# Performance work log

Hardware: AMD Instinct MI355X
Metric: run time of the kernel (lower is better)

The kernel has to match this reference:

```python
import jax, jax.numpy as jnp
import numpy as np

N = 16384        # num_variables
C = 512          # number of budget constraints
K = 64           # variables per constraint (uniform constraint_sizes)
STRIDE = 32      # overlapping windows -> every variable has degree 2
BATCH = 64
BUDGET = 8.0     # budgets[i]
MAX_ITER = 25    # ADMM / AD3 iterations
RHO = 1.0        # penalty parameter
BISECT = 25      # bisection steps for the budget projection threshold


def setup_inputs() -> dict:
    key = jax.random.key(0)
    scores = jax.random.normal(key, (BATCH, N), dtype=jnp.float32)
    # constraint_sets: constraint c covers variables [c*STRIDE, c*STRIDE+K) mod N
    base = (np.arange(C)[:, None] * STRIDE + np.arange(K)[None, :]) % N
    constraint_idx = jnp.asarray(base, dtype=jnp.int32)  # [C, K]
    return {"scores": scores, "constraint_idx": constraint_idx}


def _proj_budget(a, budget):
    """Project rows a[..., K] onto {z in [0,1]^K : sum(z) <= budget}."""
    z0 = jnp.clip(a, 0.0, 1.0)
    feasible = jnp.sum(z0, -1, keepdims=True) <= budget
    # bisection for tau with sum(clip(a - tau, 0, 1)) == budget
    a_sg = jax.lax.stop_gradient(a)
    lo = jnp.min(a_sg, -1, keepdims=True) - 1.0
    hi = jnp.max(a_sg, -1, keepdims=True)
    for _ in range(BISECT):  # fixed small algorithmic loop
        mid = 0.5 * (lo + hi)
        s = jnp.sum(jnp.clip(a_sg - mid, 0.0, 1.0), -1, keepdims=True)
        lo = jnp.where(s > budget, mid, lo)
        hi = jnp.where(s > budget, hi, mid)
    tau0 = 0.5 * (lo + hi)
    # one implicit (Newton) correction so tau is differentiable in a
    active = ((a_sg - tau0 > 0.0) & (a_sg - tau0 < 1.0)).astype(a.dtype)
    n_act = jnp.maximum(jnp.sum(active, -1, keepdims=True), 1.0)
    g = jnp.sum(jnp.clip(a - tau0, 0.0, 1.0), -1, keepdims=True) - budget
    tau = tau0 + g / n_act
    z_proj = jnp.clip(a - tau, 0.0, 1.0)
    return jnp.where(feasible, z0, z_proj)


def _forward(scores, constraint_idx):
    B, n_vars = scores.shape
    idx = constraint_idx  # [C, K]
    deg = jnp.zeros((n_vars,), scores.dtype).at[idx.reshape(-1)].add(1.0)
    deg_safe = jnp.maximum(deg, 1.0)

    def u_update(z, lam):
        # u = (theta + A^T(rho*z - lam)) / (rho * deg), boxed to [0,1]
        msg = RHO * z - lam                                   # [B,C,K]
        t = jnp.zeros_like(scores).at[:, idx].add(msg)        # A^T scatter
        u = (scores + t) / (RHO * deg_safe)
        u = jnp.clip(u, 0.0, 1.0)
        # unconstrained variables: LP optimum is the indicator of theta > 0
        return jnp.where(deg > 0.0, u, (scores > 0.0).astype(scores.dtype))

    def step(carry, _):
        z, lam = carry
        u = u_update(z, lam)
        Au = u[:, idx]                                        # gather [B,C,K]
        z_new = _proj_budget(Au + lam / RHO, BUDGET)
        lam_new = lam + RHO * (Au - z_new)
        return (z_new, lam_new), None

    z0 = jnp.zeros((B, idx.shape[0], idx.shape[1]), scores.dtype)
    lam0 = jnp.zeros_like(z0)
    (z, lam), _ = jax.lax.scan(step, (z0, lam0), None, length=MAX_ITER)
    return u_update(z, lam)


def reference(scores, constraint_idx):
    return _forward(scores, constraint_idx)
```

## Files before the change

kernel.cpp:

```cpp
#include <hip/hip_runtime.h>
#include <math.h>


#define NGLOB   16384
#define KD      64
#define MAXIT   25
#define NBIS    11
#define BUDGETF 8.0f
#define CHUNK   128
#define HALO    25
#define NCREAL  (CHUNK + 2*HALO)
#define NROWP   192
#define NTHREADS 768
#define MSGROWS (NROWP + 2)
#define RS4     17
#define OFF4    (MSGROWS * RS4)

typedef float v4f __attribute__((ext_vector_type(4)));
typedef float v2f __attribute__((ext_vector_type(2)));

__device__ __forceinline__ float clip01(float x) {
    return __builtin_amdgcn_fmed3f(x, 0.0f, 1.0f);
}
__device__ __forceinline__ v4f clipv(v4f x) {
    v4f r;
    r.x = clip01(x.x); r.y = clip01(x.y); r.z = clip01(x.z); r.w = clip01(x.w);
    return r;
}
__device__ __forceinline__ v4f minv(v4f a, v4f b) {
    v4f r; r.x=fminf(a.x,b.x); r.y=fminf(a.y,b.y); r.z=fminf(a.z,b.z); r.w=fminf(a.w,b.w); return r;
}
__device__ __forceinline__ v4f maxv(v4f a, v4f b) {
    v4f r; r.x=fmaxf(a.x,b.x); r.y=fmaxf(a.y,b.y); r.z=fmaxf(a.z,b.z); r.w=fmaxf(a.w,b.w); return r;
}
__device__ __forceinline__ float sum16(v4f a, v4f b, v4f c, v4f d) {
    v4f t = (a + b) + (c + d);
    v2f u = t.xy + t.zw;
    return u.x + u.y;
}
__device__ __forceinline__ float min16(v4f a, v4f b, v4f c, v4f d) {
    v4f t = minv(minv(a, b), minv(c, d));
    return fminf(fminf(t.x, t.y), fminf(t.z, t.w));
}
__device__ __forceinline__ float max16(v4f a, v4f b, v4f c, v4f d) {
    v4f t = maxv(maxv(a, b), maxv(c, d));
    return fmaxf(fmaxf(t.x, t.y), fmaxf(t.z, t.w));
}
__device__ __forceinline__ float ind01(float x) { return (x > 0.0f && x < 1.0f) ? 1.0f : 0.0f; }

template<int CTRL>
__device__ __forceinline__ float dpp_mv(float x) {
    union U { float f; int i; } s, r;
    s.f = x;
    r.i = __builtin_amdgcn_update_dpp(0, s.i, CTRL, 0xf, 0xf, true);
    return r.f;
}
__device__ __forceinline__ float g4_sum(float x) {
    x += dpp_mv<0xB1>(x);
    x += dpp_mv<0x4E>(x);
    return x;
}
__device__ __forceinline__ float g4_min(float x) {
    x = fminf(x, dpp_mv<0xB1>(x));
    x = fminf(x, dpp_mv<0x4E>(x));
    return x;
}
__device__ __forceinline__ float g4_max(float x) {
    x = fmaxf(x, dpp_mv<0xB1>(x));
    x = fmaxf(x, dpp_mv<0x4E>(x));
    return x;
}

__global__ void __launch_bounds__(NTHREADS, 3)
lpsmap_kernel(const float* __restrict__ scores, float* __restrict__ out) {
    __shared__ float msg[2 * OFF4 * 4];
    v4f* msg4 = (v4f*)msg;

    const int tid  = threadIdx.x;
    const int wid  = tid >> 6;
    const int lane = tid & 63;
    const int g    = lane >> 2;
    const int l4   = lane & 3;
    const int khi  = l4 >> 1;
    const int lc   = l4 & 1;
    const int b    = blockIdx.x >> 2;
    const int c0v  = (blockIdx.x & 3) * (CHUNK * 32);
    const float* sb = scores + b * NGLOB;

    for (int i = tid; i < 2 * OFF4; i += NTHREADS)
        msg4[i] = v4f{0.0f, 0.0f, 0.0f, 0.0f};

    const int rr = wid * 16 + g;
    const int i1 = (rr + khi + 1) * RS4 + 4 * lc;
    const int i2 = (rr + khi) * RS4 + 8 + 4 * lc;
    const int iw = (rr + 1) * RS4 + 4 * l4;

    v4f sch[4], lam[4], av[4];
    {
        const int off = (c0v - HALO * 32 + rr * 32 + 16 * l4 + NGLOB) & (NGLOB - 1);
        const v4f* gp = (const v4f*)(sb + off);
        #pragma unroll
        for (int q = 0; q < 4; ++q) {
            sch[q] = gp[q] * 0.5f;
            lam[q] = v4f{0.0f, 0.0f, 0.0f, 0.0f};
        }
    }

    __syncthreads();

    int roff = 0;
    #pragma unroll 1
    for (int it = 0; it < MAXIT; ++it) {
        const v4f* mr = msg4 + roff;
        v4f*       mw = msg4 + (roff ^ OFF4);

        #pragma unroll
        for (int q = 0; q < 4; ++q) {
            v4f m1 = mr[i1 + q];
            v4f m2 = mr[i2 + q];
            v4f u  = clipv((m1 + m2) * 0.5f + sch[q]);
            av[q]  = u + lam[q];
        }

        float lo = g4_min(min16(av[0], av[1], av[2], av[3])) - 1.0f;
        float hi = g4_max(max16(av[0], av[1], av[2], av[3]));

        #pragma unroll 1
        for (int j = 0; j < NBIS; ++j) {
            float mid = 0.5f * (lo + hi);
            float s = g4_sum(sum16(clipv(av[0] - mid), clipv(av[1] - mid),
                                   clipv(av[2] - mid), clipv(av[3] - mid)));
            bool gt = s > BUDGETF;
            lo = gt ? mid : lo;
            hi = gt ? hi : mid;
        }

        {
            float tau0 = 0.5f * (lo + hi);
            v4f d0 = av[0] - tau0, d1 = av[1] - tau0;
            v4f d2 = av[2] - tau0, d3 = av[3] - tau0;
            float gs = g4_sum(sum16(clipv(d0), clipv(d1), clipv(d2), clipv(d3))) - BUDGETF;
            float act = (((ind01(d0.x) + ind01(d0.y)) + (ind01(d0.z) + ind01(d0.w)))
                       + ((ind01(d1.x) + ind01(d1.y)) + (ind01(d1.z) + ind01(d1.w))))
                      + (((ind01(d2.x) + ind01(d2.y)) + (ind01(d2.z) + ind01(d2.w)))
                       + ((ind01(d3.x) + ind01(d3.y)) + (ind01(d3.z) + ind01(d3.w))));
            float nact = fmaxf(g4_sum(act), 1.0f);
            float tau = tau0 + gs * __builtin_amdgcn_rcpf(nact);
            tau = fmaxf(tau, 0.0f);
            #pragma unroll
            for (int q = 0; q < 4; ++q) {
                v4f z  = clipv(av[q] - tau);
                lam[q] = av[q] - z;
                mw[iw + q] = 2.0f * z - av[q];
            }
        }
        roff ^= OFF4;
        __syncthreads();
    }

    if (tid < CHUNK * 32 / 8) {
        const v4f* mr = msg4 + roff;
        const int j   = tid * 8;
        const int vl  = HALO * 32 + j;
        const int rrl = vl >> 5;
        const int cq  = (vl & 31) >> 2;
        v4f m1a = mr[(rrl + 1) * RS4 + cq],   m1b = mr[(rrl + 1) * RS4 + cq + 1];
        v4f m2a = mr[rrl * RS4 + 8 + cq],     m2b = mr[rrl * RS4 + 8 + cq + 1];
        const v4f* gp = (const v4f*)(sb + c0v + j);
        v4f u0 = clipv((gp[0] + m1a + m2a) * 0.5f);
        v4f u1 = clipv((gp[1] + m1b + m2b) * 0.5f);
        v4f* op = (v4f*)(out + (size_t)b * NGLOB + c0v + j);
        op[0] = u0;
        op[1] = u1;
    }
}

extern "C" void kernel_launch(void* const* d_in, const int* in_sizes, int n_in,
                              void* d_out, int out_size, void* d_ws, size_t ws_size,
                              hipStream_t stream) {
    const float* scores = (const float*)d_in[0];
    float* out = (float*)d_out;
    dim3 grid(64 * 4);
    dim3 block(NTHREADS);
    lpsmap_kernel<<<grid, block, 0, stream>>>(scores, out);
}
```

Before: 135.2 us.

## Exchange ADMM messages between lanes with ds_bpermute, shared memory only at wave edges

Each thread now keeps its own outgoing message in registers. It gets the overlapping neighbour's message through ds_bpermute lane shuffles instead of writing and reading a full double-buffered shared-memory message array. Only the edge lanes of each wave publish to and read from a small shared buffer, which cuts LDS traffic and footprint per iteration. The final output pass is also changed to use the same register-plus-shuffle path. bpermute still goes through the LDS crossbar, and the edge lanes are indexed in an intricate way.

Result: slower. 139.0 us (+2.8%).

```diff
diff --git a/kernel.cpp b/kernel.cpp
--- a/kernel.cpp
+++ b/kernel.cpp
@@ -3,18 +3,15 @@
 
 
 #define NGLOB   16384
-#define KD      64
 #define MAXIT   25
 #define NBIS    11
 #define BUDGETF 8.0f
 #define CHUNK   128
 #define HALO    25
-#define NCREAL  (CHUNK + 2*HALO)
-#define NROWP   192
 #define NTHREADS 768
-#define MSGROWS (NROWP + 2)
-#define RS4     17
-#define OFF4    (MSGROWS * RS4)
+#define NW      12
+#define PSLOTS  (NW + 2)
+#define PUBV    (PSLOTS * 2 * 2 * 4)
 
 typedef float v4f __attribute__((ext_vector_type(4)));
 typedef float v2f __attribute__((ext_vector_type(2)));
@@ -70,56 +67,68 @@
     x = fmaxf(x, dpp_mv<0x4E>(x));
     return x;
 }
+__device__ __forceinline__ v4f bperm4(int addr, v4f x) {
+    union { v4f v; int i[4]; } a, r;
+    a.v = x;
+    #pragma unroll
+    for (int t = 0; t < 4; ++t)
+        r.i[t] = __builtin_amdgcn_ds_bpermute(addr, a.i[t]);
+    return r.v;
+}
 
 __global__ void __launch_bounds__(NTHREADS, 3)
 lpsmap_kernel(const float* __restrict__ scores, float* __restrict__ out) {
-    __shared__ float msg[2 * OFF4 * 4];
-    v4f* msg4 = (v4f*)msg;
+    __shared__ v4f pub[2 * PUBV];
 
     const int tid  = threadIdx.x;
     const int wid  = tid >> 6;
     const int lane = tid & 63;
     const int g    = lane >> 2;
     const int l4   = lane & 3;
-    const int khi  = l4 >> 1;
-    const int lc   = l4 & 1;
     const int b    = blockIdx.x >> 2;
     const int c0v  = (blockIdx.x & 3) * (CHUNK * 32);
     const float* sb = scores + b * NGLOB;
 
-    for (int i = tid; i < 2 * OFF4; i += NTHREADS)
-        msg4[i] = v4f{0.0f, 0.0f, 0.0f, 0.0f};
+    if (tid < 2 * PUBV) pub[tid] = v4f{0.0f, 0.0f, 0.0f, 0.0f};
 
     const int rr = wid * 16 + g;
-    const int i1 = (rr + khi + 1) * RS4 + 4 * lc;
-    const int i2 = (rr + khi) * RS4 + 8 + 4 * lc;
-    const int iw = (rr + 1) * RS4 + 4 * l4;
+    const int bp_addr = ((((l4 < 2) ? (lane - 2) : (lane + 2)) & 63) << 2);
+    const bool edge = (lane < 2) || (lane >= 62);
+    const int l2 = lane & 1;
+    const int ridx = ((((lane < 2) ? wid : (wid + 2)) * 2 + ((lane < 2) ? 1 : 0)) * 2 + l2) * 4;
+    const int widx = (((wid + 1) * 2 + ((lane >= 62) ? 1 : 0)) * 2 + l2) * 4;
 
-    v4f sch[4], lam[4], av[4];
+    v4f sch[4], lam[4], av[4], msgr[4];
     {
         const int off = (c0v - HALO * 32 + rr * 32 + 16 * l4 + NGLOB) & (NGLOB - 1);
         const v4f* gp = (const v4f*)(sb + off);
         #pragma unroll
         for (int q = 0; q < 4; ++q) {
-            sch[q] = gp[q] * 0.5f;
-            lam[q] = v4f{0.0f, 0.0f, 0.0f, 0.0f};
+            sch[q]  = gp[q] * 0.5f;
+            lam[q]  = v4f{0.0f, 0.0f, 0.0f, 0.0f};
+            msgr[q] = v4f{0.0f, 0.0f, 0.0f, 0.0f};
         }
     }
 
     __syncthreads();
 
-    int roff = 0;
     #pragma unroll 1
     for (int it = 0; it < MAXIT; ++it) {
-        const v4f* mr = msg4 + roff;
-        v4f*       mw = msg4 + (roff ^ OFF4);
+        const v4f* pr = pub + (1 - (it & 1)) * PUBV;
+        v4f*       pw = pub + (it & 1) * PUBV;
+
+        v4f nb[4];
+        #pragma unroll
+        for (int q = 0; q < 4; ++q) nb[q] = bperm4(bp_addr, msgr[q]);
+        if (edge) {
+            #pragma unroll
+            for (int q = 0; q < 4; ++q) nb[q] = pr[ridx + q];
+        }
 
         #pragma unroll
         for (int q = 0; q < 4; ++q) {
-            v4f m1 = mr[i1 + q];
-            v4f m2 = mr[i2 + q];
-            v4f u  = clipv((m1 + m2) * 0.5f + sch[q]);
-            av[q]  = u + lam[q];
+            v4f u = clipv((msgr[q] + nb[q]) * 0.5f + sch[q]);
+            av[q] = u + lam[q];
         }
 
         float lo = g4_min(min16(av[0], av[1], av[2], av[3])) - 1.0f;
@@ -149,29 +158,33 @@
             tau = fmaxf(tau, 0.0f);
             #pragma unroll
             for (int q = 0; q < 4; ++q) {
-                v4f z  = clipv(av[q] - tau);
-                lam[q] = av[q] - z;
-                mw[iw + q] = 2.0f * z - av[q];
+                v4f z   = clipv(av[q] - tau);
+                lam[q]  = av[q] - z;
+                msgr[q] = 2.0f * z - av[q];
             }
         }
-        roff ^= OFF4;
+        if (edge) {
+            #pragma unroll
+            for (int q = 0; q < 4; ++q) pw[widx + q] = msgr[q];
+        }
         __syncthreads();
     }
 
-    if (tid < CHUNK * 32 / 8) {
-        const v4f* mr = msg4 + roff;
-        const int j   = tid * 8;
-        const int vl  = HALO * 32 + j;
-        const int rrl = vl >> 5;
-        const int cq  = (vl & 31) >> 2;
-        v4f m1a = mr[(rrl + 1) * RS4 + cq],   m1b = mr[(rrl + 1) * RS4 + cq + 1];
-        v4f m2a = mr[rrl * RS4 + 8 + cq],     m2b = mr[rrl * RS4 + 8 + cq + 1];
-        const v4f* gp = (const v4f*)(sb + c0v + j);
-        v4f u0 = clipv((gp[0] + m1a + m2a) * 0.5f);
-        v4f u1 = clipv((gp[1] + m1b + m2b) * 0.5f);
-        v4f* op = (v4f*)(out + (size_t)b * NGLOB + c0v + j);
-        op[0] = u0;
-        op[1] = u1;
+    {
+        const v4f* pr = pub + ((MAXIT - 1) & 1) * PUBV;
+        v4f nb[4];
+        #pragma unroll
+        for (int q = 0; q < 4; ++q) nb[q] = bperm4(bp_addr, msgr[q]);
+        if (edge) {
+            #pragma unroll
+            for (int q = 0; q < 4; ++q) nb[q] = pr[ridx + q];
+        }
+        if (l4 < 2 && rr >= HALO && rr < HALO + CHUNK) {
+            v4f* op = (v4f*)(out + (size_t)b * NGLOB + c0v + (rr - HALO) * 32 + 16 * l4);
+            #pragma unroll
+            for (int q = 0; q < 4; ++q)
+                op[q] = clipv((msgr[q] + nb[q]) * 0.5f + sch[q]);
+        }
     }
 }
 
```
